# Kernel tuning notes

Measured on AMD Instinct MI355X. Metric: run time of the kernel, lower is better.

The kernel has to match this reference:

```python
import jax, jax.numpy as jnp
import numpy as np

D_MODEL = 2048
N_HEAD = 16
SEM_DIM = 1024
GEO_DIM = 1024
ATTN_DIM = 2048
ROPE_BASE = 10000.0


def _rope(x, base=ROPE_BASE):
    # x: [B, H, S, d] with even d; GPT-NeoX rotate-half convention
    S, d = x.shape[-2], x.shape[-1]
    inv_freq = 1.0 / (base ** (jnp.arange(0, d, 2, dtype=jnp.float32) / d))
    t = jnp.arange(S, dtype=jnp.float32)
    freqs = jnp.einsum('s,f->sf', t, inv_freq)  # [S, d/2]
    cos, sin = jnp.cos(freqs), jnp.sin(freqs)
    x1, x2 = x[..., : d // 2], x[..., d // 2 :]
    return jnp.concatenate([x1 * cos - x2 * sin, x1 * sin + x2 * cos], axis=-1).astype(x.dtype)


def _split_heads(y, H):
    B, S, dim = y.shape
    return y.reshape(B, S, H, dim // H).transpose(0, 2, 1, 3)  # [B,H,S,hd]


def setup_inputs() -> dict:
    key = jax.random.key(0)
    ks = jax.random.split(key, 7)
    B, S = 2, 2048
    sd = 0.02
    return {
        'x': jax.random.normal(ks[0], (B, S, D_MODEL), dtype=jnp.float32),
        'Wq_sem': jax.random.normal(ks[1], (SEM_DIM, D_MODEL), dtype=jnp.float32) * sd,
        'Wk_sem': jax.random.normal(ks[2], (SEM_DIM, D_MODEL), dtype=jnp.float32) * sd,
        'Wq_geo': jax.random.normal(ks[3], (GEO_DIM, D_MODEL), dtype=jnp.float32) * sd,
        'Wk_geo': jax.random.normal(ks[4], (GEO_DIM, D_MODEL), dtype=jnp.float32) * sd,
        'Wv': jax.random.normal(ks[5], (ATTN_DIM, D_MODEL), dtype=jnp.float32) * sd,
        'Wo': jax.random.normal(ks[6], (D_MODEL, ATTN_DIM), dtype=jnp.float32) * sd,
    }


def reference(x, Wq_sem, Wk_sem, Wq_geo, Wk_geo, Wv, Wo):
    B, S, _ = x.shape
    H = N_HEAD
    # decoupled projections (nn.Linear: y = x @ W.T)
    q_sem = _split_heads(x @ Wq_sem.T, H)  # [B,H,S,64]
    k_sem = _split_heads(x @ Wk_sem.T, H)
    q_geo = _rope(_split_heads(x @ Wq_geo.T, H))  # RoPE only on geo part
    k_geo = _rope(_split_heads(x @ Wk_geo.T, H))
    v = _split_heads(x @ Wv.T, H)  # [B,H,S,128]
    # concatenated decoupled q/k -> single fused score (fp32), SDPA default scale
    q = jnp.concatenate([q_sem, q_geo], axis=-1)
    k = jnp.concatenate([k_sem, k_geo], axis=-1)
    scale = 1.0 / jnp.sqrt(jnp.asarray(q.shape[-1], dtype=jnp.float32))
    scores = jnp.einsum('bhqd,bhkd->bhqk', q, k).astype(jnp.float32) * scale
    causal = jnp.tril(jnp.ones((S, S), dtype=bool))
    scores = jnp.where(causal, scores, jnp.finfo(jnp.float32).min)
    attn = jax.nn.softmax(scores, axis=-1).astype(v.dtype)
    out = jnp.einsum('bhqk,bhkd->bhqd', attn, v)  # [B,H,S,128]
    out = out.transpose(0, 2, 1, 3).reshape(B, S, ATTN_DIM)
    return out @ Wo.T  # [B,S,d_model]
```

## Files before the change

kernel.cpp:

```cpp
#include <hip/hip_runtime.h>
#include <cstdint>
#include <cstddef>

typedef unsigned short u16;
typedef __attribute__((ext_vector_type(8))) short bf16x8;
typedef __attribute__((ext_vector_type(4))) float f32x4;

#define MFMA32(a, b, c) __builtin_amdgcn_mfma_f32_16x16x32_bf16(a, b, c, 0, 0, 0)

__device__ __forceinline__ u16 f2b(float f) {
  union { float f; unsigned u; } v; v.f = f;
  unsigned u = v.u;
  return (u16)((u + 0x7fffu + ((u >> 16) & 1u)) >> 16);
}
__device__ __forceinline__ float b2f(u16 h) {
  union { unsigned u; float f; } v; v.u = ((unsigned)h) << 16;
  return v.f;
}

__device__ __forceinline__ void g2l16(const void* g, void* l) {
  __builtin_amdgcn_global_load_lds((__attribute__((address_space(1))) void*)(g),
                                   (__attribute__((address_space(3))) void*)(l), 16, 0, 0);
}

__global__ __launch_bounds__(256) void cast_f2b_v4(const float* __restrict__ in,
                                                   u16* __restrict__ out, int n4) {
  int i = blockIdx.x * 256 + threadIdx.x;
  if (i >= n4) return;
  float4 v = ((const float4*)in)[i];
  ushort4 r;
  r.x = f2b(v.x); r.y = f2b(v.y); r.z = f2b(v.z); r.w = f2b(v.w);
  ((ushort4*)out)[i] = r;
}

__global__ __launch_bounds__(256) void cast_weights(const float* __restrict__ W0,
                                                    const float* __restrict__ W1,
                                                    const float* __restrict__ W2,
                                                    const float* __restrict__ W3,
                                                    const float* __restrict__ Wv,
                                                    const float* __restrict__ Wo,
                                                    u16* __restrict__ Wall,
                                                    u16* __restrict__ Wob) {
  const int blk = blockIdx.x;
  const float* src;
  u16* dst;
  int li;
  if (blk < 8192) {
    const int s = blk >> 11;
    src = s == 0 ? W0 : s == 1 ? W1 : s == 2 ? W2 : W3;
    dst = Wall + (size_t)s * 2097152;
    li = (blk & 2047) * 256 + threadIdx.x;
  } else if (blk < 12288) {
    src = Wv;
    dst = Wall + (size_t)4 * 2097152;
    li = (blk - 8192) * 256 + threadIdx.x;
  } else {
    src = Wo;
    dst = Wob;
    li = (blk - 12288) * 256 + threadIdx.x;
  }
  float4 v = ((const float4*)src)[li];
  ushort4 r;
  r.x = f2b(v.x); r.y = f2b(v.y); r.z = f2b(v.z); r.w = f2b(v.w);
  ((ushort4*)dst)[li] = r;
}

template <bool BF16_OUT>
__global__ __launch_bounds__(256) void gemm_bt(const u16* __restrict__ A,
                                               const u16* __restrict__ B,
                                               void* __restrict__ C, int N, int K) {
  __shared__ u16 As[128 * 64];
  __shared__ u16 Bs[128 * 64];
  const int tid = threadIdx.x;
  const int wid = tid >> 6;
  const int lane = tid & 63;
  const int lm = lane & 15;
  const int quad = lane >> 4;
  const int r3 = lm & 7;
  const int wm = (wid & 1) * 64;
  const int wn = (wid >> 1) * 64;
  const int bm = blockIdx.y * 128;
  const int bn = blockIdx.x * 128;

  const u16* Ab = A + (size_t)bm * K;
  const u16* Bb = B + (size_t)bn * K;

  f32x4 zero = {0.f, 0.f, 0.f, 0.f};
  f32x4 acc[4][4];
#pragma unroll
  for (int i = 0; i < 4; ++i)
#pragma unroll
    for (int j = 0; j < 4; ++j) acc[i][j] = zero;

  for (int k0 = 0; k0 < K; k0 += 64) {
#pragma unroll
    for (int it = 0; it < 4; ++it) {
      int c = it * 256 + tid;
      int rg = c >> 6, rw = (c >> 3) & 7, u = c & 7;
      int row = rg * 8 + rw;
      int chd = u ^ rw;
      g2l16(Ab + (size_t)row * K + k0 + chd * 8, As + c * 8);
      g2l16(Bb + (size_t)row * K + k0 + chd * 8, Bs + c * 8);
    }
    __syncthreads();
#pragma unroll
    for (int ks = 0; ks < 2; ++ks) {
      bf16x8 a[4], b[4];
      int chd = ks * 4 + quad;
#pragma unroll
      for (int i = 0; i < 4; ++i) {
        int row = wm + i * 16 + lm;
        a[i] = *(const bf16x8*)(As + (((row >> 3) * 64 + r3 * 8 + (chd ^ r3)) * 8));
      }
#pragma unroll
      for (int j = 0; j < 4; ++j) {
        int row = wn + j * 16 + lm;
        b[j] = *(const bf16x8*)(Bs + (((row >> 3) * 64 + r3 * 8 + (chd ^ r3)) * 8));
      }
#pragma unroll
      for (int i = 0; i < 4; ++i)
#pragma unroll
        for (int j = 0; j < 4; ++j)
          acc[i][j] = MFMA32(a[i], b[j], acc[i][j]);
    }
    __syncthreads();
  }

#pragma unroll
  for (int i = 0; i < 4; ++i)
#pragma unroll
    for (int j = 0; j < 4; ++j)
#pragma unroll
      for (int r = 0; r < 4; ++r) {
        int row = bm + wm + i * 16 + quad * 4 + r;
        int col = bn + wn + j * 16 + lm;
        float v = acc[i][j][r];
        if (BF16_OUT)
          ((u16*)C)[(size_t)row * N + col] = f2b(v);
        else
          ((float*)C)[(size_t)row * N + col] = v;
      }
}

__global__ __launch_bounds__(256) void gemm_qkv(const u16* __restrict__ A,
                                                const u16* __restrict__ B,
                                                u16* __restrict__ Qb,
                                                u16* __restrict__ Kb,
                                                u16* __restrict__ VT) {
  constexpr int K = 2048;
  const float SC = 0.12751744f;
  __shared__ u16 sh[16384];
  u16* As = sh;
  u16* Bs = sh + 8192;
  const int tid = threadIdx.x;
  const int wid = tid >> 6;
  const int lane = tid & 63;
  const int lm = lane & 15;
  const int quad = lane >> 4;
  const int r3 = lm & 7;
  const int wm = (wid & 1) * 64;
  const int wn = (wid >> 1) * 64;
  const int bm = blockIdx.y * 128;
  const int bn = blockIdx.x * 128;

  const u16* Ab = A + (size_t)bm * K;
  const u16* Bb = B + (size_t)bn * K;

  f32x4 zero = {0.f, 0.f, 0.f, 0.f};
  f32x4 acc[4][4];
#pragma unroll
  for (int i = 0; i < 4; ++i)
#pragma unroll
    for (int j = 0; j < 4; ++j) acc[i][j] = zero;

  for (int k0 = 0; k0 < K; k0 += 64) {
#pragma unroll
    for (int it = 0; it < 4; ++it) {
      int c = it * 256 + tid;
      int rg = c >> 6, rw = (c >> 3) & 7, u = c & 7;
      int row = rg * 8 + rw;
      int chd = u ^ rw;
      g2l16(Ab + (size_t)row * K + k0 + chd * 8, As + c * 8);
      g2l16(Bb + (size_t)row * K + k0 + chd * 8, Bs + c * 8);
    }
    __syncthreads();
#pragma unroll
    for (int ks = 0; ks < 2; ++ks) {
      bf16x8 a[4], b[4];
      int chd = ks * 4 + quad;
#pragma unroll
      for (int i = 0; i < 4; ++i) {
        int row = wm + i * 16 + lm;
        a[i] = *(const bf16x8*)(As + (((row >> 3) * 64 + r3 * 8 + (chd ^ r3)) * 8));
      }
#pragma unroll
      for (int j = 0; j < 4; ++j) {
        int row = wn + j * 16 + lm;
        b[j] = *(const bf16x8*)(Bs + (((row >> 3) * 64 + r3 * 8 + (chd ^ r3)) * 8));
      }
#pragma unroll
      for (int i = 0; i < 4; ++i)
#pragma unroll
        for (int j = 0; j < 4; ++j)
          acc[i][j] = MFMA32(a[i], b[j], acc[i][j]);
    }
    __syncthreads();
  }

  const int seg = bn >> 10;
  const int b = bm >> 11;
  const int sbase = bm & 2047;
  const int h = ((bn + wn) >> 6) & 15;
  const size_t bhQ = (size_t)b * 16 + h;

  if (seg < 2) {
    u16* dst = (seg == 0) ? Qb : Kb;
    const float sc = (seg == 0) ? SC : 1.0f;
#pragma unroll
    for (int i = 0; i < 4; ++i)
#pragma unroll
      for (int r = 0; r < 4; ++r) {
        const int s = sbase + wm + i * 16 + quad * 4 + r;
        u16* base = dst + (bhQ * 2048 + s) * 128;
#pragma unroll
        for (int j = 0; j < 4; ++j) {
          const int d = (wn + j * 16 + lm) & 63;
          base[d] = f2b(acc[i][j][r] * sc);
        }
      }
  } else if (seg < 4) {
    u16* dst = (seg == 2) ? Qb : Kb;
    const float sc = (seg == 2) ? SC : 1.0f;
    const float inv0 = __powf(10000.0f, -(float)(2 * lm) * (1.0f / 64.0f));
    const float inv1 = __powf(10000.0f, -(float)(2 * (16 + lm)) * (1.0f / 64.0f));
#pragma unroll
    for (int i = 0; i < 4; ++i)
#pragma unroll
      for (int r = 0; r < 4; ++r) {
        const int s = sbase + wm + i * 16 + quad * 4 + r;
        float sn0, cs0, sn1, cs1;
        __sincosf((float)s * inv0, &sn0, &cs0);
        __sincosf((float)s * inv1, &sn1, &cs1);
        const float x1a = acc[i][0][r], x2a = acc[i][2][r];
        const float x1b = acc[i][1][r], x2b = acc[i][3][r];
        u16* base = dst + (bhQ * 2048 + s) * 128 + 64;
        base[lm]      = f2b((x1a * cs0 - x2a * sn0) * sc);
        base[16 + lm] = f2b((x1b * cs1 - x2b * sn1) * sc);
        base[32 + lm] = f2b((x1a * sn0 + x2a * cs0) * sc);
        base[48 + lm] = f2b((x1b * sn1 + x2b * cs1) * sc);
      }
  } else {
    const int hv = (bn - 4096) >> 7;
    const size_t bh = (size_t)b * 16 + hv;
    u16(*buf)[66] = (u16(*)[66])sh;
    const int myhalf = wn >> 6;
#pragma unroll 1
    for (int half = 0; half < 2; ++half) {
      __syncthreads();
      if (myhalf == half) {
#pragma unroll
        for (int i = 0; i < 4; ++i)
#pragma unroll
          for (int j = 0; j < 4; ++j)
#pragma unroll
            for (int r = 0; r < 4; ++r)
              buf[wm + i * 16 + quad * 4 + r][j * 16 + lm] = f2b(acc[i][j][r]);
      }
      __syncthreads();
#pragma unroll
      for (int it = 0; it < 8; ++it) {
        const int idx = it * 256 + tid;
        const int dd = idx >> 5;
        const int sc4 = idx & 31;
        ushort4 v;
        v.x = buf[sc4 * 4 + 0][dd];
        v.y = buf[sc4 * 4 + 1][dd];
        v.z = buf[sc4 * 4 + 2][dd];
        v.w = buf[sc4 * 4 + 3][dd];
        *(ushort4*)(VT + (bh * 128 + half * 64 + dd) * 2048 + sbase + sc4 * 4) = v;
      }
    }
  }
}

__global__ __launch_bounds__(256, 2) void attn_v8(const u16* __restrict__ Q,
                                                  const u16* __restrict__ K,
                                                  const u16* __restrict__ VT,
                                                  u16* __restrict__ O) {
  constexpr int S = 2048;
  constexpr int D = 128;
  __shared__ u16 Ks[2][64 * 128];
  __shared__ u16 Vs[2][128 * 64];
  __shared__ u16 Ps[64 * 72];
  const int linear = blockIdx.x + (blockIdx.y << 4);
  const int xcd = linear & 7;
  const int slot = linear >> 3;
  const int bh = (xcd << 2) + (slot >> 4);
  const int bx = slot & 15;
  const int b = bh >> 4, h = bh & 15;
  const int tid = threadIdx.x, wid = tid >> 6, lane = tid & 63;
  const int lm = lane & 15, quad = lane >> 4;
  const int rx = lm & 7;
  const int wrow = wid * 16;

  const u16* Kbh = K + (size_t)bh * S * D;
  const u16* Vbh = VT + (size_t)bh * D * S;

  auto stageKV = [&](int kt, int bufid) {
    const u16* Kt = Kbh + (size_t)kt * 64 * D;
    const u16* Vt = Vbh + (size_t)kt * 64;
#pragma unroll
    for (int it = 0; it < 4; ++it) {
      int c = it * 256 + tid;
      int row = c >> 4, u = c & 15;
      g2l16(Kt + (size_t)row * 128 + (size_t)(u ^ (row & 7)) * 8, &Ks[bufid][c * 8]);
    }
#pragma unroll
    for (int it = 0; it < 4; ++it) {
      int c = it * 256 + tid;
      int row = c >> 3, u = c & 7;
      g2l16(Vt + (size_t)row * S + (size_t)(u ^ (row & 7)) * 8, &Vs[bufid][c * 8]);
    }
  };

#pragma unroll 1
  for (int pass = 0; pass < 2; ++pass) {
    const int qt = pass == 0 ? bx : 31 - bx;

    bf16x8 aq[4];
#pragma unroll
    for (int ks = 0; ks < 4; ++ks)
      aq[ks] = *(const bf16x8*)(Q + ((size_t)bh * S + (size_t)qt * 64 + wrow + lm) * D +
                                ks * 32 + quad * 8);

    float l_r[4] = {0.f, 0.f, 0.f, 0.f};
    f32x4 zero = {0.f, 0.f, 0.f, 0.f};
    f32x4 oacc[8];
#pragma unroll
    for (int t = 0; t < 8; ++t) oacc[t] = zero;

    stageKV(0, 0);
    asm volatile("s_waitcnt vmcnt(0)" ::: "memory");
    __builtin_amdgcn_s_barrier();

#pragma unroll 1
    for (int kt = 0; kt <= qt; ++kt) {
      const int cur = kt & 1;
      if (kt < qt) stageKV(kt + 1, cur ^ 1);

      f32x4 sc[4];
#pragma unroll
      for (int j = 0; j < 4; ++j) sc[j] = zero;
      __builtin_amdgcn_s_setprio(1);
#pragma unroll
      for (int ks = 0; ks < 4; ++ks) {
        const int kc = ks * 4 + quad;
#pragma unroll
        for (int j = 0; j < 4; ++j) {
          bf16x8 bk = *(const bf16x8*)(&Ks[cur][((j * 16 + lm) * 16 + (kc ^ rx)) * 8]);
          sc[j] = MFMA32(aq[ks], bk, sc[j]);
        }
      }
      __builtin_amdgcn_s_setprio(0);

      const bool diag = (kt == qt);
#pragma unroll
      for (int r = 0; r < 4; ++r) {
        const int qcol = wrow + quad * 4 + r;
        float pv[4];
        float rs = 0.f;
#pragma unroll
        for (int j = 0; j < 4; ++j) {
          float p = __builtin_amdgcn_exp2f(fminf(sc[j][r], 30.0f));
          if (diag && (j * 16 + lm > qcol)) p = 0.f;
          rs += p;
          pv[j] = p;
        }
#pragma unroll
        for (int dd = 1; dd < 16; dd <<= 1) rs += __shfl_xor(rs, dd);
        l_r[r] += rs;
        const int prow = (wrow + quad * 4 + r) * 72;
#pragma unroll
        for (int j = 0; j < 4; ++j) Ps[prow + j * 16 + lm] = f2b(pv[j]);
      }

      __builtin_amdgcn_s_setprio(1);
#pragma unroll
      for (int ks = 0; ks < 2; ++ks) {
        bf16x8 ap = *(const bf16x8*)(Ps + (wrow + lm) * 72 + ks * 32 + quad * 8);
        const int kc = ks * 4 + quad;
#pragma unroll
        for (int t = 0; t < 8; ++t) {
          bf16x8 bv = *(const bf16x8*)(&Vs[cur][((t * 16 + lm) * 8 + (kc ^ rx)) * 8]);
          oacc[t] = MFMA32(ap, bv, oacc[t]);
        }
      }
      __builtin_amdgcn_s_setprio(0);

      if (kt < qt) asm volatile("s_waitcnt vmcnt(0)" ::: "memory");
      __builtin_amdgcn_s_barrier();
    }

#pragma unroll
    for (int r = 0; r < 4; ++r) {
      float inv = 1.0f / l_r[r];
      const int srow = qt * 64 + wrow + quad * 4 + r;
      u16* Orow = O + ((size_t)b * S + srow) * 2048 + h * 128;
#pragma unroll
      for (int t = 0; t < 8; ++t) Orow[t * 16 + lm] = f2b(oacc[t][r] * inv);
    }
  }
}

extern "C" void kernel_launch(void* const* d_in, const int* in_sizes, int n_in,
                              void* d_out, int out_size, void* d_ws, size_t ws_size,
                              hipStream_t stream) {
  const float* x      = (const float*)d_in[0];
  const float* Wq_sem = (const float*)d_in[1];
  const float* Wk_sem = (const float*)d_in[2];
  const float* Wq_geo = (const float*)d_in[3];
  const float* Wk_geo = (const float*)d_in[4];
  const float* Wv     = (const float*)d_in[5];
  const float* Wo     = (const float*)d_in[6];

  char* ws = (char*)d_ws;
  u16* xb   = (u16*)(ws);
  u16* Wall = (u16*)(ws + 16777216);
  u16* Wob  = (u16*)(ws + 16777216 + 25165824);
  u16* Qb   = (u16*)(ws + 16777216 + 25165824 + 8388608);
  u16* Ob   = Wall;
  u16* Kb   = (u16*)d_out;
  u16* VT   = (u16*)((char*)d_out + 16777216);

  cast_f2b_v4<<<8192, 256, 0, stream>>>(x, xb, 2097152);
  cast_weights<<<16384, 256, 0, stream>>>(Wq_sem, Wk_sem, Wq_geo, Wk_geo, Wv, Wo, Wall, Wob);

  gemm_qkv<<<dim3(48, 32), 256, 0, stream>>>(xb, Wall, Qb, Kb, VT);

  attn_v8<<<dim3(16, 32), 256, 0, stream>>>(Qb, Kb, VT, Ob);

  gemm_bt<false><<<dim3(16, 32), 256, 0, stream>>>(Ob, Wob, d_out, 2048, 2048);
}
```

Before: 373.2 us.

## Merge cast kernels, swizzle V transpose, single-buffer attention with MFMA row sums

Merges the x and weight casts into one launch. Replaces the two-pass padded V transpose in the QKV GEMM epilogue with a single XOR-swizzled LDS transpose that does 16-byte stores. Changes the attention kernel from double-buffered to single-buffered K/V, which cuts LDS so three blocks can fit per CU. It also computes softmax row sums with an extra MFMA against a ones vector instead of shuffle reductions. The trade is that attention no longer overlaps the next tile's loads with compute, and the row sums now come from bf16-rounded probabilities.

Result: faster. 359.4 us (median of 2 runs) (-3.7%).

```diff
diff --git a/kernel.cpp b/kernel.cpp
--- a/kernel.cpp
+++ b/kernel.cpp
@@ -23,41 +23,33 @@
                                    (__attribute__((address_space(3))) void*)(l), 16, 0, 0);
 }
 
-__global__ __launch_bounds__(256) void cast_f2b_v4(const float* __restrict__ in,
-                                                   u16* __restrict__ out, int n4) {
-  int i = blockIdx.x * 256 + threadIdx.x;
-  if (i >= n4) return;
-  float4 v = ((const float4*)in)[i];
-  ushort4 r;
-  r.x = f2b(v.x); r.y = f2b(v.y); r.z = f2b(v.z); r.w = f2b(v.w);
-  ((ushort4*)out)[i] = r;
-}
-
-__global__ __launch_bounds__(256) void cast_weights(const float* __restrict__ W0,
-                                                    const float* __restrict__ W1,
-                                                    const float* __restrict__ W2,
-                                                    const float* __restrict__ W3,
-                                                    const float* __restrict__ Wv,
-                                                    const float* __restrict__ Wo,
-                                                    u16* __restrict__ Wall,
-                                                    u16* __restrict__ Wob) {
+__global__ __launch_bounds__(256) void cast_all(const float* __restrict__ x,
+                                                const float* __restrict__ W0,
+                                                const float* __restrict__ W1,
+                                                const float* __restrict__ W2,
+                                                const float* __restrict__ W3,
+                                                const float* __restrict__ Wv,
+                                                const float* __restrict__ Wo,
+                                                u16* __restrict__ xb,
+                                                u16* __restrict__ Wall,
+                                                u16* __restrict__ Wob) {
   const int blk = blockIdx.x;
   const float* src;
   u16* dst;
   int li;
   if (blk < 8192) {
-    const int s = blk >> 11;
+    src = x; dst = xb; li = blk * 256 + threadIdx.x;
+  } else if (blk < 16384) {
+    const int s = (blk - 8192) >> 11;
     src = s == 0 ? W0 : s == 1 ? W1 : s == 2 ? W2 : W3;
     dst = Wall + (size_t)s * 2097152;
-    li = (blk & 2047) * 256 + threadIdx.x;
-  } else if (blk < 12288) {
-    src = Wv;
-    dst = Wall + (size_t)4 * 2097152;
-    li = (blk - 8192) * 256 + threadIdx.x;
+    li = ((blk - 8192) & 2047) * 256 + threadIdx.x;
+  } else if (blk < 20480) {
+    src = Wv; dst = Wall + (size_t)4 * 2097152;
+    li = (blk - 16384) * 256 + threadIdx.x;
   } else {
-    src = Wo;
-    dst = Wob;
-    li = (blk - 12288) * 256 + threadIdx.x;
+    src = Wo; dst = Wob;
+    li = (blk - 20480) * 256 + threadIdx.x;
   }
   float4 v = ((const float4*)src)[li];
   ushort4 r;
@@ -252,45 +244,37 @@
   } else {
     const int hv = (bn - 4096) >> 7;
     const size_t bh = (size_t)b * 16 + hv;
-    u16(*buf)[66] = (u16(*)[66])sh;
-    const int myhalf = wn >> 6;
-#pragma unroll 1
-    for (int half = 0; half < 2; ++half) {
-      __syncthreads();
-      if (myhalf == half) {
-#pragma unroll
-        for (int i = 0; i < 4; ++i)
-#pragma unroll
-          for (int j = 0; j < 4; ++j)
-#pragma unroll
-            for (int r = 0; r < 4; ++r)
-              buf[wm + i * 16 + quad * 4 + r][j * 16 + lm] = f2b(acc[i][j][r]);
-      }
-      __syncthreads();
-#pragma unroll
-      for (int it = 0; it < 8; ++it) {
-        const int idx = it * 256 + tid;
-        const int dd = idx >> 5;
-        const int sc4 = idx & 31;
-        ushort4 v;
-        v.x = buf[sc4 * 4 + 0][dd];
-        v.y = buf[sc4 * 4 + 1][dd];
-        v.z = buf[sc4 * 4 + 2][dd];
-        v.w = buf[sc4 * 4 + 3][dd];
-        *(ushort4*)(VT + (bh * 128 + half * 64 + dd) * 2048 + sbase + sc4 * 4) = v;
-      }
+#pragma unroll
+    for (int i = 0; i < 4; ++i)
+#pragma unroll
+      for (int r = 0; r < 4; ++r) {
+        const int sr = wm + i * 16 + quad * 4 + r;
+#pragma unroll
+        for (int j = 0; j < 4; ++j) {
+          const int d = wn + j * 16 + lm;
+          sh[d * 128 + (((sr >> 3) ^ (d & 7)) << 3) + (sr & 7)] = f2b(acc[i][j][r]);
+        }
+      }
+    __syncthreads();
+#pragma unroll
+    for (int it = 0; it < 8; ++it) {
+      const int idx = it * 256 + tid;
+      const int d = idx >> 4;
+      const int ch = idx & 15;
+      bf16x8 v = *(const bf16x8*)(sh + d * 128 + ((ch ^ (d & 7)) << 3));
+      *(bf16x8*)(VT + (bh * 128 + d) * 2048 + sbase + ch * 8) = v;
     }
   }
 }
 
-__global__ __launch_bounds__(256, 2) void attn_v8(const u16* __restrict__ Q,
+__global__ __launch_bounds__(256, 3) void attn_v9(const u16* __restrict__ Q,
                                                   const u16* __restrict__ K,
                                                   const u16* __restrict__ VT,
                                                   u16* __restrict__ O) {
   constexpr int S = 2048;
   constexpr int D = 128;
-  __shared__ u16 Ks[2][64 * 128];
-  __shared__ u16 Vs[2][128 * 64];
+  __shared__ u16 Ks[64 * 128];
+  __shared__ u16 Vs[128 * 64];
   __shared__ u16 Ps[64 * 72];
   const int linear = blockIdx.x + (blockIdx.y << 4);
   const int xcd = linear & 7;
@@ -306,22 +290,7 @@
   const u16* Kbh = K + (size_t)bh * S * D;
   const u16* Vbh = VT + (size_t)bh * D * S;
 
-  auto stageKV = [&](int kt, int bufid) {
-    const u16* Kt = Kbh + (size_t)kt * 64 * D;
-    const u16* Vt = Vbh + (size_t)kt * 64;
-#pragma unroll
-    for (int it = 0; it < 4; ++it) {
-      int c = it * 256 + tid;
-      int row = c >> 4, u = c & 15;
-      g2l16(Kt + (size_t)row * 128 + (size_t)(u ^ (row & 7)) * 8, &Ks[bufid][c * 8]);
-    }
-#pragma unroll
-    for (int it = 0; it < 4; ++it) {
-      int c = it * 256 + tid;
-      int row = c >> 3, u = c & 7;
-      g2l16(Vt + (size_t)row * S + (size_t)(u ^ (row & 7)) * 8, &Vs[bufid][c * 8]);
-    }
-  };
+  const bf16x8 vones = {16256, 16256, 16256, 16256, 16256, 16256, 16256, 16256};
 
 #pragma unroll 1
   for (int pass = 0; pass < 2; ++pass) {
@@ -333,20 +302,30 @@
       aq[ks] = *(const bf16x8*)(Q + ((size_t)bh * S + (size_t)qt * 64 + wrow + lm) * D +
                                 ks * 32 + quad * 8);
 
-    float l_r[4] = {0.f, 0.f, 0.f, 0.f};
     f32x4 zero = {0.f, 0.f, 0.f, 0.f};
+    f32x4 lsum = zero;
     f32x4 oacc[8];
 #pragma unroll
     for (int t = 0; t < 8; ++t) oacc[t] = zero;
-
-    stageKV(0, 0);
-    asm volatile("s_waitcnt vmcnt(0)" ::: "memory");
-    __builtin_amdgcn_s_barrier();
 
 #pragma unroll 1
     for (int kt = 0; kt <= qt; ++kt) {
-      const int cur = kt & 1;
-      if (kt < qt) stageKV(kt + 1, cur ^ 1);
+      __syncthreads();
+      const u16* Kt = Kbh + (size_t)kt * 64 * D;
+      const u16* Vt = Vbh + (size_t)kt * 64;
+#pragma unroll
+      for (int it = 0; it < 4; ++it) {
+        int c = it * 256 + tid;
+        int row = c >> 4, u = c & 15;
+        g2l16(Kt + (size_t)row * 128 + (size_t)(u ^ (row & 7)) * 8, Ks + c * 8);
+      }
+#pragma unroll
+      for (int it = 0; it < 4; ++it) {
+        int c = it * 256 + tid;
+        int row = c >> 3, u = c & 7;
+        g2l16(Vt + (size_t)row * S + (size_t)(u ^ (row & 7)) * 8, Vs + c * 8);
+      }
+      __syncthreads();
 
       f32x4 sc[4];
 #pragma unroll
@@ -357,7 +336,7 @@
         const int kc = ks * 4 + quad;
 #pragma unroll
         for (int j = 0; j < 4; ++j) {
-          bf16x8 bk = *(const bf16x8*)(&Ks[cur][((j * 16 + lm) * 16 + (kc ^ rx)) * 8]);
+          bf16x8 bk = *(const bf16x8*)(Ks + (((j * 16 + lm) * 16 + (kc ^ rx)) * 8));
           sc[j] = MFMA32(aq[ks], bk, sc[j]);
         }
       }
@@ -367,21 +346,13 @@
 #pragma unroll
       for (int r = 0; r < 4; ++r) {
         const int qcol = wrow + quad * 4 + r;
-        float pv[4];
-        float rs = 0.f;
+        const int prow = (wrow + quad * 4 + r) * 72;
 #pragma unroll
         for (int j = 0; j < 4; ++j) {
           float p = __builtin_amdgcn_exp2f(fminf(sc[j][r], 30.0f));
           if (diag && (j * 16 + lm > qcol)) p = 0.f;
-          rs += p;
-          pv[j] = p;
+          Ps[prow + j * 16 + lm] = f2b(p);
         }
-#pragma unroll
-        for (int dd = 1; dd < 16; dd <<= 1) rs += __shfl_xor(rs, dd);
-        l_r[r] += rs;
-        const int prow = (wrow + quad * 4 + r) * 72;
-#pragma unroll
-        for (int j = 0; j < 4; ++j) Ps[prow + j * 16 + lm] = f2b(pv[j]);
       }
 
       __builtin_amdgcn_s_setprio(1);
@@ -389,21 +360,19 @@
       for (int ks = 0; ks < 2; ++ks) {
         bf16x8 ap = *(const bf16x8*)(Ps + (wrow + lm) * 72 + ks * 32 + quad * 8);
         const int kc = ks * 4 + quad;
+        lsum = MFMA32(ap, vones, lsum);
 #pragma unroll
         for (int t = 0; t < 8; ++t) {
-          bf16x8 bv = *(const bf16x8*)(&Vs[cur][((t * 16 + lm) * 8 + (kc ^ rx)) * 8]);
+          bf16x8 bv = *(const bf16x8*)(Vs + (((t * 16 + lm) * 8 + (kc ^ rx)) * 8));
           oacc[t] = MFMA32(ap, bv, oacc[t]);
         }
       }
       __builtin_amdgcn_s_setprio(0);
-
-      if (kt < qt) asm volatile("s_waitcnt vmcnt(0)" ::: "memory");
-      __builtin_amdgcn_s_barrier();
     }
 
 #pragma unroll
     for (int r = 0; r < 4; ++r) {
-      float inv = 1.0f / l_r[r];
+      float inv = 1.0f / lsum[r];
       const int srow = qt * 64 + wrow + quad * 4 + r;
       u16* Orow = O + ((size_t)b * S + srow) * 2048 + h * 128;
 #pragma unroll
@@ -432,12 +401,12 @@
   u16* Kb   = (u16*)d_out;
   u16* VT   = (u16*)((char*)d_out + 16777216);
 
-  cast_f2b_v4<<<8192, 256, 0, stream>>>(x, xb, 2097152);
-  cast_weights<<<16384, 256, 0, stream>>>(Wq_sem, Wk_sem, Wq_geo, Wk_geo, Wv, Wo, Wall, Wob);
+  cast_all<<<24576, 256, 0, stream>>>(x, Wq_sem, Wk_sem, Wq_geo, Wk_geo, Wv, Wo,
+                                      xb, Wall, Wob);
 
   gemm_qkv<<<dim3(48, 32), 256, 0, stream>>>(xb, Wall, Qb, Kb, VT);
 
-  attn_v8<<<dim3(16, 32), 256, 0, stream>>>(Qb, Kb, VT, Ob);
+  attn_v9<<<dim3(16, 32), 256, 0, stream>>>(Qb, Kb, VT, Ob);
 
   gemm_bt<false><<<dim3(16, 32), 256, 0, stream>>>(Ob, Wob, d_out, 2048, 2048);
 }
```
